# Optimization experiments

Hardware: AMD Instinct MI355X
Metric: run time of the kernel (lower is better)

Reference implementation:

```python
import jax, jax.numpy as jnp
import numpy as np

B, N, C1 = 4, 4096, 58
K = 32
RADIUS = 0.3
CIN = C1 + 6  # xyz(3) + centered grouped_xyz(3) + feature(C1)
OUT_DIMS = [64, 64, 128]
EPS = 1e-5


def setup_inputs() -> dict:
    key = jax.random.key(0)
    ks = jax.random.split(key, 8)
    inp = {
        "feature": jax.random.normal(ks[0], (B, N, C1), dtype=jnp.float32),
        "xyz": jax.random.uniform(ks[1], (B, N, 3), dtype=jnp.float32),
    }
    dims = [CIN] + OUT_DIMS
    for i in range(len(OUT_DIMS)):
        inp[f"W{i}"] = jax.random.normal(ks[2 + i], (dims[i + 1], dims[i]), dtype=jnp.float32) * 0.05
        inp[f"g{i}"] = jnp.ones((dims[i + 1],), dtype=jnp.float32)
        inp[f"b{i}"] = jnp.zeros((dims[i + 1],), dtype=jnp.float32)
    return inp


def ball_query(xyz, radius, k):
    # xyz: (B,N,3) -> grouped neighbor indices (B,N,K), repo semantics:
    # indices with dist > radius set to N, sorted, first K taken, pads replaced by first valid index.
    n = xyz.shape[1]
    sq = jnp.sum((xyz[:, :, None, :] - xyz[:, None, :, :]) ** 2, axis=-1)  # (B,N,N)
    ar = jnp.arange(n, dtype=jnp.int32)[None, None, :]
    inds = jnp.where(sq > radius * radius, n, ar)
    inds = jnp.sort(inds, axis=-1)[:, :, :k]  # (B,N,K)
    first = inds[:, :, :1]
    return jnp.where(inds == n, first, inds)


def group_norm(x, gamma, beta, groups):
    # x: (B,C,K,N); normalize per (group of channels x all spatial)
    b, c, k, n = x.shape
    xg = x.reshape(b, groups, -1)
    mu = jnp.mean(xg, axis=-1, keepdims=True)
    var = jnp.var(xg, axis=-1, keepdims=True)
    xg = (xg - mu) * jax.lax.rsqrt(var + EPS)
    x = xg.reshape(b, c, k, n)
    return x * gamma[None, :, None, None] + beta[None, :, None, None]


def reference(feature, xyz, W0, g0, b0, W1, g1, b1, W2, g2, b2):
    inds = ball_query(xyz, RADIUS, K)  # (B,N,K) int
    gather = jax.vmap(lambda arr, idx: arr[idx])  # per-batch fancy gather
    grouped_xyz = gather(xyz, inds) - xyz[:, :, None, :]        # (B,N,K,3) centered
    grouped_feat = gather(feature, inds)                        # (B,N,K,C1)
    center = jnp.broadcast_to(xyz[:, :, None, :], (B, N, K, 3))  # repeated query xyz
    new_points = jnp.concatenate([center, grouped_xyz, grouped_feat], axis=-1)  # (B,N,K,CIN)

    x = new_points  # layout handled inside einsum: torch permute(0,3,2,1) -> (B,C,K,N)
    params = [(W0, g0, b0), (W1, g1, b1), (W2, g2, b2)]
    first = True
    for (w, g, b_), od in zip(params, OUT_DIMS):
        if first:
            x = jnp.einsum('bnkc,oc->bokn', x, w)  # conv1x1, no bias
            first = False
        else:
            x = jnp.einsum('bikn,oi->bokn', x, w)
        x = group_norm(x, g, b_, od // 32)
        x = jax.nn.relu(x)
    return jnp.max(x, axis=2)  # (B, C2, N)
```

## Files before the change

### kernel.cpp

```cpp
#include <hip/hip_runtime.h>
#include <stdint.h>

#define B_ 4
#define N_ 4096
#define C1_ 58
#define K_ 32
#define EPS_ 1e-5f

typedef __attribute__((ext_vector_type(8))) short bf16x8;
typedef __attribute__((ext_vector_type(4))) float f32x4;

static __device__ __forceinline__ float bf2f(unsigned short u){
  return __uint_as_float(((unsigned int)u) << 16);
}
static __device__ __forceinline__ unsigned short f2bf(float f){
  unsigned int x = __float_as_uint(f);
  x = (x + 0x7FFFu + ((x >> 16) & 1u)) >> 16;
  return (unsigned short)x;
}
static __device__ __forceinline__ unsigned int cvt_pk_bf16(float lo, float hi){
  unsigned int r;
  asm("v_cvt_pk_bf16_f32 %0, %1, %2" : "=v"(r) : "v"(lo), "v"(hi));
  return r;
}

__global__ __launch_bounds__(256) void ball_kernel(const float* __restrict__ xyz,
                                                   int* __restrict__ inds){
  const int wid  = (blockIdx.x * 256 + threadIdx.x) >> 6;
  const int lane = threadIdx.x & 63;
  const int b = wid >> 12;
  const int n = wid & (N_ - 1);
  const float* xb = xyz + (size_t)b * N_ * 3;
  const float qx = xb[n*3+0], qy = xb[n*3+1], qz = xb[n*3+2];
  const float R2 = (float)(0.3 * 0.3);
  int* outp = inds + (size_t)wid * K_;
  int cnt = 0;
  int first = -1;
  for (int j0 = 0; j0 < N_ && cnt < K_; j0 += 64){
    const int j = j0 + lane;
    float dx = xb[j*3+0] - qx;
    float dy = xb[j*3+1] - qy;
    float dz = xb[j*3+2] - qz;
    float s = __fadd_rn(__fadd_rn(__fmul_rn(dx,dx), __fmul_rn(dy,dy)), __fmul_rn(dz,dz));
    bool p = (s <= R2);
    unsigned long long mask = __ballot(p);
    if (p){
      int pos = cnt + __popcll(mask & ((1ull << lane) - 1ull));
      if (pos < K_) outp[pos] = j;
    }
    if (first < 0 && mask) first = j0 + __builtin_ctzll(mask);
    cnt += __popcll(mask);
  }
  if (lane < K_ && lane >= cnt) outp[lane] = first;
}

__global__ __launch_bounds__(256)
void pq_kernel(const float* __restrict__ feature, const float* __restrict__ xyz,
               const float* __restrict__ W0g, const float* __restrict__ W2g,
               float* __restrict__ P, unsigned short* __restrict__ Q,
               unsigned short* __restrict__ W2bf)
{
  __shared__ float W0l[64 * 65];
  __shared__ float vql[32][64];
  const int t = threadIdx.x, bid = blockIdx.x;

  if (bid == 0){
    for (int i = t; i < 128 * 64; i += 256) W2bf[i] = f2bf(W2g[i]);
  }
  #pragma unroll
  for (int i = 0; i < 16; ++i){
    int idx = i * 256 + t;
    W0l[(idx >> 6) * 65 + (idx & 63)] = W0g[idx];
  }
  const int gpt0 = bid * 32;
  const int b = gpt0 >> 12;
  const size_t pb = (size_t)b * N_;
  #pragma unroll
  for (int i = 0; i < 8; ++i){
    int task = i * 256 + t;
    int r = task >> 6, c = task & 63;
    int n = (gpt0 + r) & (N_ - 1);
    float val = 0.f;
    if (c < 3)       val = xyz[(pb + n) * 3 + c];
    else if (c < 61) val = feature[(pb + n) * C1_ + (c - 3)];
    vql[r][c] = val;
  }
  __syncthreads();

  const int o = t & 63;
  const int r0 = t >> 6;
  #pragma unroll
  for (int it = 0; it < 8; ++it){
    int r = r0 + it * 4;
    float q0 = 0.f, q1 = 0.f;
    #pragma unroll
    for (int i = 0; i < 60; i += 2){
      q0 = fmaf(W0l[o*65 + 3 + i],     vql[r][i],     q0);
      q1 = fmaf(W0l[o*65 + 3 + i + 1], vql[r][i + 1], q1);
    }
    q0 = fmaf(W0l[o*65 + 3 + 60], vql[r][60], q0);
    float qv = q0 + q1;
    float p = 0.f;
    #pragma unroll
    for (int c = 0; c < 3; ++c)
      p = fmaf(W0l[o*65 + c] - W0l[o*65 + c + 3], vql[r][c], p);
    size_t gpt = (size_t)gpt0 + r;
    P[gpt * 64 + o] = p;
    Q[gpt * 64 + o] = f2bf(qv);
  }
}

__global__ __launch_bounds__(256)
void stats0_kernel(const int* __restrict__ inds, const float* __restrict__ P,
                   const unsigned short* __restrict__ Q, float* __restrict__ partials)
{
  const int t = threadIdx.x, bid = blockIdx.x;
  const size_t row0 = (size_t)bid * 1024;
  const int c8 = t & 7;
  float s = 0.f, q = 0.f;
  for (int i = 0; i < 32; ++i){
    size_t task = (size_t)i * 256 + t;
    size_t row = row0 + (task >> 3);
    int idx = inds[row];
    size_t pt = row >> 5;
    size_t qpt = ((row >> 17) << 12) + idx;
    const float4* pp = (const float4*)(P + pt * 64 + c8 * 8);
    float4 pa = pp[0], pb = pp[1];
    bf16x8 qv = *(const bf16x8*)(Q + qpt * 64 + c8 * 8);
    float pv[8] = {pa.x, pa.y, pa.z, pa.w, pb.x, pb.y, pb.z, pb.w};
    #pragma unroll
    for (int j = 0; j < 8; ++j){
      float y = pv[j] + bf2f((unsigned short)qv[j]);
      s += y; q = fmaf(y, y, q);
    }
  }
  s += __shfl_xor(s, 1, 64);  q += __shfl_xor(q, 1, 64);
  s += __shfl_xor(s, 2, 64);  q += __shfl_xor(q, 2, 64);
  s += __shfl_xor(s, 8, 64);  q += __shfl_xor(q, 8, 64);
  s += __shfl_xor(s, 16, 64); q += __shfl_xor(q, 16, 64);
  s += __shfl_xor(s, 32, 64); q += __shfl_xor(q, 32, 64);
  const int lane = t & 63, w = t >> 6;
  float* out = partials + ((size_t)bid * 4 + w) * 4;
  if (lane == 0){ out[0] = s; out[1] = q; }
  if (lane == 4){ out[2] = s; out[3] = q; }
}

template<int DEPTH>
__global__ __launch_bounds__(512)
void conv_chain(const int* __restrict__ inds, const float* __restrict__ P,
                const unsigned short* __restrict__ Q,
                const float* __restrict__ sc0, const float* __restrict__ sb0,
                const float* __restrict__ W1g, const unsigned short* __restrict__ W2bf,
                const float* __restrict__ sc1, const float* __restrict__ sb1,
                float* __restrict__ partials, float* __restrict__ ymax,
                float* __restrict__ ymin)
{
  constexpr int TILES = 4;
  constexpr int NGF = (DEPTH == 2) ? 4 : 2;
  constexpr int NG2 = NGF * 2;
  __shared__ unsigned short W1l[64 * 64];
  __shared__ unsigned short Xl[2][256 * 64];
  __shared__ float spart[8][NG2];

  const int t = threadIdx.x, bid = blockIdx.x;
  const size_t blk_row0 = (size_t)bid * 1024;
  const int b = bid >> 7;
  const int lane = t & 63, w = t >> 6;
  const int col = lane & 15, quad = lane >> 4;
  const int c8 = t & 7;

  float s0r[8], b0r[8];
  #pragma unroll
  for (int j = 0; j < 8; ++j){
    s0r[j] = sc0[b * 64 + c8 * 8 + j];
    b0r[j] = sb0[b * 64 + c8 * 8 + j];
  }
  float s1r[4], b1r[4];
  if constexpr (DEPTH == 2){
    #pragma unroll
    for (int nt = 0; nt < 4; ++nt){
      s1r[nt] = sc1[b * 64 + nt * 16 + col];
      b1r[nt] = sb1[b * 64 + nt * 16 + col];
    }
  }

  {
    int ch = t >> 3, c = t & 7;
    const float* wr = W1g + ch * 64 + c * 8;
    bf16x8 v;
    #pragma unroll
    for (int j = 0; j < 8; ++j) v[j] = (short)f2bf(wr[j]);
    *(bf16x8*)&W1l[ch * 64 + ((c ^ (ch & 7)) * 8)] = v;
  }

  int    idxr[4];
  bf16x8 qvr[4];

  auto issue = [&](int tile){
    const size_t row0 = blk_row0 + (size_t)tile * 256;
    #pragma unroll
    for (int i = 0; i < 4; ++i)
      idxr[i] = inds[row0 + ((i * 512 + t) >> 3)];
    #pragma unroll
    for (int i = 0; i < 4; ++i){
      size_t qpt = ((size_t)b << 12) + idxr[i];
      qvr[i] = *(const bf16x8*)(Q + qpt * 64 + c8 * 8);
    }
  };

  auto writeT = [&](int tile, int buf){
    const size_t row0 = blk_row0 + (size_t)tile * 256;
    #pragma unroll
    for (int i = 0; i < 4; ++i){
      int r = (i * 512 + t) >> 3;
      size_t pt = (row0 + r) >> 5;
      const float4* pp = (const float4*)(P + pt * 64 + c8 * 8);
      float4 pa = pp[0], pb = pp[1];
      float pv[8] = {pa.x, pa.y, pa.z, pa.w, pb.x, pb.y, pb.z, pb.w};
      float a[8];
      #pragma unroll
      for (int j = 0; j < 8; ++j){
        float y = pv[j] + bf2f((unsigned short)qvr[i][j]);
        float v = fmaf(y, s0r[j], b0r[j]);
        a[j] = fmaxf(v, 0.f);
      }
      unsigned int pk[4];
      #pragma unroll
      for (int j = 0; j < 4; ++j) pk[j] = cvt_pk_bf16(a[2*j], a[2*j+1]);
      unsigned int* dst = (unsigned int*)&Xl[buf][r * 64 + ((c8 ^ (r & 7)) * 8)];
      #pragma unroll
      for (int j = 0; j < 4; ++j) dst[j] = pk[j];
    }
  };

  float sg[NGF], qg[NGF];
  #pragma unroll
  for (int g = 0; g < NGF; ++g){ sg[g] = 0.f; qg[g] = 0.f; }

  issue(0);
  writeT(0, 0);

  for (int tile = 0; tile < TILES; ++tile){
    const int cur = tile & 1;
    const size_t row0 = blk_row0 + (size_t)tile * 256;
    __syncthreads();
    if (tile + 1 < TILES) issue(tile + 1);

    float cmx[(DEPTH == 2) ? 8 : 1], cmn[(DEPTH == 2) ? 8 : 1];
    if constexpr (DEPTH == 2){
      #pragma unroll
      for (int nt = 0; nt < 8; ++nt){ cmx[nt] = -1e30f; cmn[nt] = 1e30f; }
    }

    #pragma unroll
    for (int mi = 0; mi < 2; ++mi){
      const int r = w * 32 + mi * 16 + col;
      bf16x8 afr[2];
      #pragma unroll
      for (int kt = 0; kt < 2; ++kt)
        afr[kt] = *(const bf16x8*)&Xl[cur][r * 64 + (((kt * 4 + quad) ^ (r & 7)) * 8)];
      f32x4 acc1[4];
      #pragma unroll
      for (int nt = 0; nt < 4; ++nt) acc1[nt] = (f32x4){0.f,0.f,0.f,0.f};
      #pragma unroll
      for (int kt = 0; kt < 2; ++kt)
        #pragma unroll
        for (int nt = 0; nt < 4; ++nt){
          int ch = nt * 16 + col;
          bf16x8 bfr = *(const bf16x8*)&W1l[ch * 64 + (((kt * 4 + quad) ^ (ch & 7)) * 8)];
          acc1[nt] = __builtin_amdgcn_mfma_f32_16x16x32_bf16(afr[kt], bfr, acc1[nt], 0, 0, 0);
        }

      if constexpr (DEPTH == 1){
        #pragma unroll
        for (int nt = 0; nt < 4; ++nt)
          #pragma unroll
          for (int rg = 0; rg < 4; ++rg){
            float y = acc1[nt][rg];
            sg[nt >> 1] += y;
            qg[nt >> 1] = fmaf(y, y, qg[nt >> 1]);
          }
      } else {
        #pragma unroll
        for (int nt = 0; nt < 4; ++nt)
          #pragma unroll
          for (int rg = 0; rg < 4; ++rg){
            int rr = w * 32 + mi * 16 + quad * 4 + rg;
            int ch = nt * 16 + col;
            float v = fmaf(acc1[nt][rg], s1r[nt], b1r[nt]);
            v = fmaxf(v, 0.f);
            Xl[cur][rr * 64 + (((ch >> 3) ^ (rr & 7)) * 8) + (ch & 7)] = f2bf(v);
          }
        bf16x8 a2f[2];
        #pragma unroll
        for (int kt = 0; kt < 2; ++kt)
          a2f[kt] = *(const bf16x8*)&Xl[cur][r * 64 + (((kt * 4 + quad) ^ (r & 7)) * 8)];
        f32x4 acc2[8];
        #pragma unroll
        for (int nt = 0; nt < 8; ++nt) acc2[nt] = (f32x4){0.f,0.f,0.f,0.f};
        #pragma unroll
        for (int kt = 0; kt < 2; ++kt)
          #pragma unroll
          for (int nt = 0; nt < 8; ++nt){
            int ch = nt * 16 + col;
            bf16x8 bfr = *(const bf16x8*)&W2bf[ch * 64 + (kt * 4 + quad) * 8];
            acc2[nt] = __builtin_amdgcn_mfma_f32_16x16x32_bf16(a2f[kt], bfr, acc2[nt], 0, 0, 0);
          }
        #pragma unroll
        for (int nt = 0; nt < 8; ++nt)
          #pragma unroll
          for (int rg = 0; rg < 4; ++rg){
            float y = acc2[nt][rg];
            sg[nt >> 1] += y;
            qg[nt >> 1] = fmaf(y, y, qg[nt >> 1]);
            cmx[nt] = fmaxf(cmx[nt], y);
            cmn[nt] = fminf(cmn[nt], y);
          }
      }
    }

    if constexpr (DEPTH == 2){
      #pragma unroll
      for (int nt = 0; nt < 8; ++nt){
        cmx[nt] = fmaxf(cmx[nt], __shfl_xor(cmx[nt], 16, 64));
        cmx[nt] = fmaxf(cmx[nt], __shfl_xor(cmx[nt], 32, 64));
        cmn[nt] = fminf(cmn[nt], __shfl_xor(cmn[nt], 16, 64));
        cmn[nt] = fminf(cmn[nt], __shfl_xor(cmn[nt], 32, 64));
      }
      if (quad == 0){
        size_t pt = (row0 >> 5) + w;
        #pragma unroll
        for (int nt = 0; nt < 8; ++nt){
          ymax[pt * 128 + nt * 16 + col] = cmx[nt];
          ymin[pt * 128 + nt * 16 + col] = cmn[nt];
        }
      }
    }

    if (tile + 1 < TILES) writeT(tile + 1, cur ^ 1);
  }

  #pragma unroll
  for (int g = 0; g < NGF; ++g){
    #pragma unroll
    for (int off = 32; off > 0; off >>= 1){
      sg[g] += __shfl_down(sg[g], off, 64);
      qg[g] += __shfl_down(qg[g], off, 64);
    }
  }
  if (lane == 0){
    #pragma unroll
    for (int g = 0; g < NGF; ++g){
      spart[w][g * 2 + 0] = sg[g];
      spart[w][g * 2 + 1] = qg[g];
    }
  }
  __syncthreads();
  if (t < NG2){
    float v = 0.f;
    #pragma unroll
    for (int ww = 0; ww < 8; ++ww) v += spart[ww][t];
    partials[(size_t)bid * NG2 + t] = v;
  }
}

template<int NCH, int NPER>
__global__ __launch_bounds__(256)
void finalize_kernel(const float* __restrict__ partials,
                     const float* __restrict__ g, const float* __restrict__ bb,
                     float* __restrict__ sc, float* __restrict__ sb){
  constexpr int NG2 = (NCH / 32) * 2;
  constexpr int NSLOTS = 4 * NG2;
  constexpr int TPS = 256 / NSLOTS;
  __shared__ float st[NSLOTS];
  const int t = threadIdx.x;
  const int slot = t / TPS, j = t % TPS;
  const int b = slot / NG2, idx = slot % NG2;
  float acc = 0.f;
  #pragma unroll
  for (int i = 0; i < NPER / TPS; ++i)
    acc += partials[((size_t)b * NPER + j + i * TPS) * NG2 + idx];
  #pragma unroll
  for (int off = TPS >> 1; off > 0; off >>= 1)
    acc += __shfl_down(acc, off, 64);
  if (j == 0) st[slot] = acc;
  __syncthreads();
  for (int c0 = t; c0 < 4 * NCH; c0 += 256){
    int b2 = c0 / NCH, c = c0 % NCH, grp = c >> 5;
    float s = st[b2 * NG2 + grp * 2 + 0], q = st[b2 * NG2 + grp * 2 + 1];
    const float cnt = 4194304.f;
    float mean = s / cnt;
    float var = q / cnt - mean * mean;
    float rstd = 1.f / sqrtf(var + EPS_);
    float scale = rstd * g[c];
    sc[b2 * NCH + c] = scale;
    sb[b2 * NCH + c] = bb[c] - mean * scale;
  }
}

__global__ __launch_bounds__(256)
void out_kernel(const float* __restrict__ ymax, const float* __restrict__ ymin,
                const float* __restrict__ sc2, const float* __restrict__ sb2,
                float* __restrict__ out){
  __shared__ float tile[64 * 129];
  const int t = threadIdx.x;
  const int b = blockIdx.y;
  const int n0 = blockIdx.x * 64;
  const float4* mx4 = (const float4*)(ymax + ((size_t)b * N_ + n0) * 128);
  const float4* mn4 = (const float4*)(ymin + ((size_t)b * N_ + n0) * 128);
  #pragma unroll
  for (int i = 0; i < 8; ++i){
    int e4 = i * 256 + t;
    int nl = e4 >> 5;
    int ch0 = (e4 & 31) * 4;
    float4 vx = mx4[e4], vn = mn4[e4];
    #pragma unroll
    for (int j = 0; j < 4; ++j){
      float slope = sc2[b*128 + ch0 + j];
      float off   = sb2[b*128 + ch0 + j];
      float y = (slope >= 0.f) ? ((const float*)&vx)[j] : ((const float*)&vn)[j];
      float v = fmaf(y, slope, off);
      tile[nl*129 + ch0 + j] = v > 0.f ? v : 0.f;
    }
  }
  __syncthreads();
  const int ch = t >> 1, h = t & 1;
  float* orow = out + ((size_t)b * 128 + ch) * N_ + n0 + h * 32;
  #pragma unroll
  for (int jj = 0; jj < 8; ++jj){
    float4 v;
    #pragma unroll
    for (int c = 0; c < 4; ++c)
      ((float*)&v)[c] = tile[(h*32 + jj*4 + c)*129 + ch];
    ((float4*)orow)[jj] = v;
  }
}

extern "C" void kernel_launch(void* const* d_in, const int* in_sizes, int n_in,
                              void* d_out, int out_size, void* d_ws, size_t ws_size,
                              hipStream_t stream) {
  const float* feature = (const float*)d_in[0];
  const float* xyz     = (const float*)d_in[1];
  const float* W0 = (const float*)d_in[2];
  const float* g0 = (const float*)d_in[3];
  const float* b0 = (const float*)d_in[4];
  const float* W1 = (const float*)d_in[5];
  const float* g1 = (const float*)d_in[6];
  const float* b1 = (const float*)d_in[7];
  const float* W2 = (const float*)d_in[8];
  const float* g2 = (const float*)d_in[9];
  const float* b2 = (const float*)d_in[10];
  float* out = (float*)d_out;

  char* ws = (char*)d_ws;
  const size_t INDS_BYTES = (size_t)B_ * N_ * K_ * sizeof(int);
  const size_t YBYTES     = (size_t)B_ * N_ * 128 * sizeof(float);
  const size_t PBYTES     = (size_t)B_ * N_ * 64 * sizeof(float);
  const size_t QBYTES     = (size_t)B_ * N_ * 64 * 2;
  int* inds            = (int*)ws;
  float* ymax          = (float*)(ws + INDS_BYTES);
  float* ymin          = (float*)(ws + INDS_BYTES + YBYTES);
  float* P             = (float*)(ws + INDS_BYTES + 2 * YBYTES);
  unsigned short* Q    = (unsigned short*)(ws + INDS_BYTES + 2 * YBYTES + PBYTES);
  unsigned short* W2bf = (unsigned short*)(ws + INDS_BYTES + 2 * YBYTES + PBYTES + QBYTES);
  float* p0 = (float*)(ws + INDS_BYTES + 2 * YBYTES + PBYTES + QBYTES + 16384);
  float* p1 = p0 + 2048 * 4;
  float* p2 = p1 + 512 * 4;
  float* sc0 = p2 + 512 * 8;
  float* sb0 = sc0 + 256;
  float* sc1 = sb0 + 256;
  float* sb1 = sc1 + 256;
  float* sc2 = sb1 + 256;
  float* sb2 = sc2 + 512;

  ball_kernel<<<B_ * N_ / 4, 256, 0, stream>>>(xyz, inds);
  pq_kernel<<<B_ * N_ / 32, 256, 0, stream>>>(feature, xyz, W0, W2, P, Q, W2bf);

  stats0_kernel<<<B_ * N_ * K_ / 1024, 256, 0, stream>>>(inds, P, Q, p0);
  finalize_kernel<64, 512><<<1, 256, 0, stream>>>(p0, g0, b0, sc0, sb0);

  const int GRID = 512;

  conv_chain<1><<<GRID, 512, 0, stream>>>(
      inds, P, Q, sc0, sb0, W1, nullptr, nullptr, nullptr,
      p1, nullptr, nullptr);
  finalize_kernel<64, 128><<<1, 256, 0, stream>>>(p1, g1, b1, sc1, sb1);

  conv_chain<2><<<GRID, 512, 0, stream>>>(
      inds, P, Q, sc0, sb0, W1, W2bf, sc1, sb1,
      p2, ymax, ymin);
  finalize_kernel<128, 128><<<1, 256, 0, stream>>>(p2, g2, b2, sc2, sb2);

  dim3 ogrid(N_ / 64, B_);
  out_kernel<<<ogrid, 256, 0, stream>>>(ymax, ymin, sc2, sb2, out);
}
```

Measured before the change: 144.2 us.

## Replace multi-tile pipelined conv blocks with many small single-tile blocks

Result: slower. 162.3 us (+12.5%).

```diff
diff --git a/kernel.cpp b/kernel.cpp
--- a/kernel.cpp
+++ b/kernel.cpp
@@ -146,7 +146,7 @@
 }
 
 template<int DEPTH>
-__global__ __launch_bounds__(512)
+__global__ __launch_bounds__(256)
 void conv_chain(const int* __restrict__ inds, const float* __restrict__ P,
                 const unsigned short* __restrict__ Q,
                 const float* __restrict__ sc0, const float* __restrict__ sb0,
@@ -155,20 +155,24 @@
                 float* __restrict__ partials, float* __restrict__ ymax,
                 float* __restrict__ ymin)
 {
-  constexpr int TILES = 4;
   constexpr int NGF = (DEPTH == 2) ? 4 : 2;
   constexpr int NG2 = NGF * 2;
   __shared__ unsigned short W1l[64 * 64];
-  __shared__ unsigned short Xl[2][256 * 64];
-  __shared__ float spart[8][NG2];
+  __shared__ unsigned short Xl[128 * 64];
+  __shared__ float spart[4][NG2];
 
   const int t = threadIdx.x, bid = blockIdx.x;
-  const size_t blk_row0 = (size_t)bid * 1024;
-  const int b = bid >> 7;
+  const size_t row0 = (size_t)bid * 128;
+  const int b = bid >> 10;
   const int lane = t & 63, w = t >> 6;
   const int col = lane & 15, quad = lane >> 4;
   const int c8 = t & 7;
 
+  int idxr[4];
+  #pragma unroll
+  for (int i = 0; i < 4; ++i)
+    idxr[i] = inds[row0 + ((i * 256 + t) >> 3)];
+
   float s0r[8], b0r[8];
   #pragma unroll
   for (int j = 0; j < 8; ++j){
@@ -183,9 +187,10 @@
       b1r[nt] = sb1[b * 64 + nt * 16 + col];
     }
   }
-
-  {
-    int ch = t >> 3, c = t & 7;
+  #pragma unroll
+  for (int i = 0; i < 2; ++i){
+    int idx = i * 256 + t;
+    int ch = idx >> 3, c = idx & 7;
     const float* wr = W1g + ch * 64 + c * 8;
     bf16x8 v;
     #pragma unroll
@@ -193,151 +198,128 @@
     *(bf16x8*)&W1l[ch * 64 + ((c ^ (ch & 7)) * 8)] = v;
   }
 
-  int    idxr[4];
   bf16x8 qvr[4];
-
-  auto issue = [&](int tile){
-    const size_t row0 = blk_row0 + (size_t)tile * 256;
-    #pragma unroll
-    for (int i = 0; i < 4; ++i)
-      idxr[i] = inds[row0 + ((i * 512 + t) >> 3)];
-    #pragma unroll
-    for (int i = 0; i < 4; ++i){
-      size_t qpt = ((size_t)b << 12) + idxr[i];
-      qvr[i] = *(const bf16x8*)(Q + qpt * 64 + c8 * 8);
-    }
-  };
-
-  auto writeT = [&](int tile, int buf){
-    const size_t row0 = blk_row0 + (size_t)tile * 256;
-    #pragma unroll
-    for (int i = 0; i < 4; ++i){
-      int r = (i * 512 + t) >> 3;
-      size_t pt = (row0 + r) >> 5;
-      const float4* pp = (const float4*)(P + pt * 64 + c8 * 8);
-      float4 pa = pp[0], pb = pp[1];
-      float pv[8] = {pa.x, pa.y, pa.z, pa.w, pb.x, pb.y, pb.z, pb.w};
-      float a[8];
-      #pragma unroll
-      for (int j = 0; j < 8; ++j){
-        float y = pv[j] + bf2f((unsigned short)qvr[i][j]);
-        float v = fmaf(y, s0r[j], b0r[j]);
-        a[j] = fmaxf(v, 0.f);
+  #pragma unroll
+  for (int i = 0; i < 4; ++i){
+    size_t qpt = ((size_t)b << 12) + idxr[i];
+    qvr[i] = *(const bf16x8*)(Q + qpt * 64 + c8 * 8);
+  }
+
+  #pragma unroll
+  for (int i = 0; i < 4; ++i){
+    int r = (i * 256 + t) >> 3;
+    size_t pt = (row0 + r) >> 5;
+    const float4* pp = (const float4*)(P + pt * 64 + c8 * 8);
+    float4 pa = pp[0], pb = pp[1];
+    float pv[8] = {pa.x, pa.y, pa.z, pa.w, pb.x, pb.y, pb.z, pb.w};
+    float a[8];
+    #pragma unroll
+    for (int j = 0; j < 8; ++j){
+      float y = pv[j] + bf2f((unsigned short)qvr[i][j]);
+      float v = fmaf(y, s0r[j], b0r[j]);
+      a[j] = fmaxf(v, 0.f);
+    }
+    unsigned int pk[4];
+    #pragma unroll
+    for (int j = 0; j < 4; ++j) pk[j] = cvt_pk_bf16(a[2*j], a[2*j+1]);
+    unsigned int* dst = (unsigned int*)&Xl[r * 64 + ((c8 ^ (r & 7)) * 8)];
+    #pragma unroll
+    for (int j = 0; j < 4; ++j) dst[j] = pk[j];
+  }
+  __syncthreads();
+
+  float sg[NGF], qg[NGF];
+  #pragma unroll
+  for (int g = 0; g < NGF; ++g){ sg[g] = 0.f; qg[g] = 0.f; }
+  float cmx[(DEPTH == 2) ? 8 : 1], cmn[(DEPTH == 2) ? 8 : 1];
+  if constexpr (DEPTH == 2){
+    #pragma unroll
+    for (int nt = 0; nt < 8; ++nt){ cmx[nt] = -1e30f; cmn[nt] = 1e30f; }
+  }
+
+  #pragma unroll
+  for (int mi = 0; mi < 2; ++mi){
+    const int r = w * 32 + mi * 16 + col;
+    bf16x8 afr[2];
+    #pragma unroll
+    for (int kt = 0; kt < 2; ++kt)
+      afr[kt] = *(const bf16x8*)&Xl[r * 64 + (((kt * 4 + quad) ^ (r & 7)) * 8)];
+    f32x4 acc1[4];
+    #pragma unroll
+    for (int nt = 0; nt < 4; ++nt) acc1[nt] = (f32x4){0.f,0.f,0.f,0.f};
+    #pragma unroll
+    for (int kt = 0; kt < 2; ++kt)
+      #pragma unroll
+      for (int nt = 0; nt < 4; ++nt){
+        int ch = nt * 16 + col;
+        bf16x8 bfr = *(const bf16x8*)&W1l[ch * 64 + (((kt * 4 + quad) ^ (ch & 7)) * 8)];
+        acc1[nt] = __builtin_amdgcn_mfma_f32_16x16x32_bf16(afr[kt], bfr, acc1[nt], 0, 0, 0);
       }
-      unsigned int pk[4];
-      #pragma unroll
-      for (int j = 0; j < 4; ++j) pk[j] = cvt_pk_bf16(a[2*j], a[2*j+1]);
-      unsigned int* dst = (unsigned int*)&Xl[buf][r * 64 + ((c8 ^ (r & 7)) * 8)];
-      #pragma unroll
-      for (int j = 0; j < 4; ++j) dst[j] = pk[j];
-    }
-  };
-
-  float sg[NGF], qg[NGF];
-  #pragma unroll
-  for (int g = 0; g < NGF; ++g){ sg[g] = 0.f; qg[g] = 0.f; }
-
-  issue(0);
-  writeT(0, 0);
-
-  for (int tile = 0; tile < TILES; ++tile){
-    const int cur = tile & 1;
-    const size_t row0 = blk_row0 + (size_t)tile * 256;
-    __syncthreads();
-    if (tile + 1 < TILES) issue(tile + 1);
-
-    float cmx[(DEPTH == 2) ? 8 : 1], cmn[(DEPTH == 2) ? 8 : 1];
-    if constexpr (DEPTH == 2){
-      #pragma unroll
-      for (int nt = 0; nt < 8; ++nt){ cmx[nt] = -1e30f; cmn[nt] = 1e30f; }
-    }
-
-    #pragma unroll
-    for (int mi = 0; mi < 2; ++mi){
-      const int r = w * 32 + mi * 16 + col;
-      bf16x8 afr[2];
+
+    if constexpr (DEPTH == 1){
+      #pragma unroll
+      for (int nt = 0; nt < 4; ++nt)
+        #pragma unroll
+        for (int rg = 0; rg < 4; ++rg){
+          float y = acc1[nt][rg];
+          sg[nt >> 1] += y;
+          qg[nt >> 1] = fmaf(y, y, qg[nt >> 1]);
+        }
+    } else {
+      #pragma unroll
+      for (int nt = 0; nt < 4; ++nt)
+        #pragma unroll
+        for (int rg = 0; rg < 4; ++rg){
+          int rr = w * 32 + mi * 16 + quad * 4 + rg;
+          int ch = nt * 16 + col;
+          float v = fmaf(acc1[nt][rg], s1r[nt], b1r[nt]);
+          v = fmaxf(v, 0.f);
+          Xl[rr * 64 + (((ch >> 3) ^ (rr & 7)) * 8) + (ch & 7)] = f2bf(v);
+        }
+      bf16x8 a2f[2];
       #pragma unroll
       for (int kt = 0; kt < 2; ++kt)
-        afr[kt] = *(const bf16x8*)&Xl[cur][r * 64 + (((kt * 4 + quad) ^ (r & 7)) * 8)];
-      f32x4 acc1[4];
-      #pragma unroll
-      for (int nt = 0; nt < 4; ++nt) acc1[nt] = (f32x4){0.f,0.f,0.f,0.f};
+        a2f[kt] = *(const bf16x8*)&Xl[r * 64 + (((kt * 4 + quad) ^ (r & 7)) * 8)];
+      f32x4 acc2[8];
+      #pragma unroll
+      for (int nt = 0; nt < 8; ++nt) acc2[nt] = (f32x4){0.f,0.f,0.f,0.f};
       #pragma unroll
       for (int kt = 0; kt < 2; ++kt)
         #pragma unroll
-        for (int nt = 0; nt < 4; ++nt){
+        for (int nt = 0; nt < 8; ++nt){
           int ch = nt * 16 + col;
-          bf16x8 bfr = *(const bf16x8*)&W1l[ch * 64 + (((kt * 4 + quad) ^ (ch & 7)) * 8)];
-          acc1[nt] = __builtin_amdgcn_mfma_f32_16x16x32_bf16(afr[kt], bfr, acc1[nt], 0, 0, 0);
+          bf16x8 bfr = *(const bf16x8*)&W2bf[ch * 64 + (kt * 4 + quad) * 8];
+          acc2[nt] = __builtin_amdgcn_mfma_f32_16x16x32_bf16(a2f[kt], bfr, acc2[nt], 0, 0, 0);
         }
-
-      if constexpr (DEPTH == 1){
+      #pragma unroll
+      for (int nt = 0; nt < 8; ++nt)
         #pragma unroll
-        for (int nt = 0; nt < 4; ++nt)
-          #pragma unroll
-          for (int rg = 0; rg < 4; ++rg){
-            float y = acc1[nt][rg];
-            sg[nt >> 1] += y;
-            qg[nt >> 1] = fmaf(y, y, qg[nt >> 1]);
-          }
-      } else {
-        #pragma unroll
-        for (int nt = 0; nt < 4; ++nt)
-          #pragma unroll
-          for (int rg = 0; rg < 4; ++rg){
-            int rr = w * 32 + mi * 16 + quad * 4 + rg;
-            int ch = nt * 16 + col;
-            float v = fmaf(acc1[nt][rg], s1r[nt], b1r[nt]);
-            v = fmaxf(v, 0.f);
-            Xl[cur][rr * 64 + (((ch >> 3) ^ (rr & 7)) * 8) + (ch & 7)] = f2bf(v);
-          }
-        bf16x8 a2f[2];
-        #pragma unroll
-        for (int kt = 0; kt < 2; ++kt)
-          a2f[kt] = *(const bf16x8*)&Xl[cur][r * 64 + (((kt * 4 + quad) ^ (r & 7)) * 8)];
-        f32x4 acc2[8];
-        #pragma unroll
-        for (int nt = 0; nt < 8; ++nt) acc2[nt] = (f32x4){0.f,0.f,0.f,0.f};
-        #pragma unroll
-        for (int kt = 0; kt < 2; ++kt)
-          #pragma unroll
-          for (int nt = 0; nt < 8; ++nt){
-            int ch = nt * 16 + col;
-            bf16x8 bfr = *(const bf16x8*)&W2bf[ch * 64 + (kt * 4 + quad) * 8];
-            acc2[nt] = __builtin_amdgcn_mfma_f32_16x16x32_bf16(a2f[kt], bfr, acc2[nt], 0, 0, 0);
-          }
-        #pragma unroll
-        for (int nt = 0; nt < 8; ++nt)
-          #pragma unroll
-          for (int rg = 0; rg < 4; ++rg){
-            float y = acc2[nt][rg];
-            sg[nt >> 1] += y;
-            qg[nt >> 1] = fmaf(y, y, qg[nt >> 1]);
-            cmx[nt] = fmaxf(cmx[nt], y);
-            cmn[nt] = fminf(cmn[nt], y);
-          }
+        for (int rg = 0; rg < 4; ++rg){
+          float y = acc2[nt][rg];
+          sg[nt >> 1] += y;
+          qg[nt >> 1] = fmaf(y, y, qg[nt >> 1]);
+          cmx[nt] = fmaxf(cmx[nt], y);
+          cmn[nt] = fminf(cmn[nt], y);
+        }
+    }
+  }
+
+  if constexpr (DEPTH == 2){
+    #pragma unroll
+    for (int nt = 0; nt < 8; ++nt){
+      cmx[nt] = fmaxf(cmx[nt], __shfl_xor(cmx[nt], 16, 64));
+      cmx[nt] = fmaxf(cmx[nt], __shfl_xor(cmx[nt], 32, 64));
+      cmn[nt] = fminf(cmn[nt], __shfl_xor(cmn[nt], 16, 64));
+      cmn[nt] = fminf(cmn[nt], __shfl_xor(cmn[nt], 32, 64));
+    }
+    if (quad == 0){
+      size_t pt = (row0 >> 5) + w;
+      #pragma unroll
+      for (int nt = 0; nt < 8; ++nt){
+        ymax[pt * 128 + nt * 16 + col] = cmx[nt];
+        ymin[pt * 128 + nt * 16 + col] = cmn[nt];
       }
     }
-
-    if constexpr (DEPTH == 2){
-      #pragma unroll
-      for (int nt = 0; nt < 8; ++nt){
-        cmx[nt] = fmaxf(cmx[nt], __shfl_xor(cmx[nt], 16, 64));
-        cmx[nt] = fmaxf(cmx[nt], __shfl_xor(cmx[nt], 32, 64));
-        cmn[nt] = fminf(cmn[nt], __shfl_xor(cmn[nt], 16, 64));
-        cmn[nt] = fminf(cmn[nt], __shfl_xor(cmn[nt], 32, 64));
-      }
-      if (quad == 0){
-        size_t pt = (row0 >> 5) + w;
-        #pragma unroll
-        for (int nt = 0; nt < 8; ++nt){
-          ymax[pt * 128 + nt * 16 + col] = cmx[nt];
-          ymin[pt * 128 + nt * 16 + col] = cmn[nt];
-        }
-      }
-    }
-
-    if (tile + 1 < TILES) writeT(tile + 1, cur ^ 1);
   }
 
   #pragma unroll
@@ -357,9 +339,7 @@
   }
   __syncthreads();
   if (t < NG2){
-    float v = 0.f;
-    #pragma unroll
-    for (int ww = 0; ww < 8; ++ww) v += spart[ww][t];
+    float v = spart[0][t] + spart[1][t] + spart[2][t] + spart[3][t];
     partials[(size_t)bid * NG2 + t] = v;
   }
 }
@@ -465,8 +445,8 @@
   unsigned short* W2bf = (unsigned short*)(ws + INDS_BYTES + 2 * YBYTES + PBYTES + QBYTES);
   float* p0 = (float*)(ws + INDS_BYTES + 2 * YBYTES + PBYTES + QBYTES + 16384);
   float* p1 = p0 + 2048 * 4;
-  float* p2 = p1 + 512 * 4;
-  float* sc0 = p2 + 512 * 8;
+  float* p2 = p1 + 4096 * 4;
+  float* sc0 = p2 + 4096 * 8;
   float* sb0 = sc0 + 256;
   float* sc1 = sb0 + 256;
   float* sb1 = sc1 + 256;
@@ -479,17 +459,17 @@
   stats0_kernel<<<B_ * N_ * K_ / 1024, 256, 0, stream>>>(inds, P, Q, p0);
   finalize_kernel<64, 512><<<1, 256, 0, stream>>>(p0, g0, b0, sc0, sb0);
 
-  const int GRID = 512;
-
-  conv_chain<1><<<GRID, 512, 0, stream>>>(
+  const int GRID = B_ * N_ * K_ / 128;
+
+  conv_chain<1><<<GRID, 256, 0, stream>>>(
       inds, P, Q, sc0, sb0, W1, nullptr, nullptr, nullptr,
       p1, nullptr, nullptr);
-  finalize_kernel<64, 128><<<1, 256, 0, stream>>>(p1, g1, b1, sc1, sb1);
-
-  conv_chain<2><<<GRID, 512, 0, stream>>>(
+  finalize_kernel<64, 1024><<<1, 256, 0, stream>>>(p1, g1, b1, sc1, sb1);
+
+  conv_chain<2><<<GRID, 256, 0, stream>>>(
       inds, P, Q, sc0, sb0, W1, W2bf, sc1, sb1,
       p2, ymax, ymin);
-  finalize_kernel<128, 128><<<1, 256, 0, stream>>>(p2, g2, b2, sc2, sb2);
+  finalize_kernel<128, 1024><<<1, 256, 0, stream>>>(p2, g2, b2, sc2, sb2);
 
   dim3 ogrid(N_ / 64, B_);
   out_kernel<<<ogrid, 256, 0, stream>>>(ymax, ymin, sc2, sb2, out);
```
